# Performance work log

Measured on AMD Instinct MI355X. Metric: run time of the kernel, lower is better.

## Reference

```python
import jax, jax.numpy as jnp
import numpy as np

EPS = 1e-08


def setup_inputs() -> dict:
    key = jax.random.key(0)
    k1, k2 = jax.random.split(key)
    n, d = 8192, 64
    x = jax.random.normal(k1, (n, d), dtype=jnp.float32)
    y = jax.random.randint(k2, (n,), 0, 10, dtype=jnp.int64)
    # weights = 1 / temperature_init = 1 / 0.1
    weights = jnp.full((1,), 10.0, dtype=jnp.float32)
    return {"x": x, "y": y, "weights": weights}


def reference(x, y, weights):
    n = x.shape[0]
    # pairwise euclidean distances (torch.cdist p=2)
    sq = jnp.sum(x * x, axis=1)                      # [n]
    d2 = sq[:, None] + sq[None, :] - 2.0 * (x @ x.T)  # [n,n]
    eye = jnp.eye(n, dtype=bool)
    d2 = jnp.maximum(d2, 0.0)
    dist = jnp.where(eye, 0.0, jnp.sqrt(jnp.where(eye, 1.0, d2)))  # safe sqrt on diag
    expo = jnp.exp(-dist * weights[0])               # [n,n]
    same = (y[:, None] == y[None, :]) & ~eye         # same-class, excluding self
    top = jnp.sum(jnp.where(same, expo, 0.0), axis=1)  # [n]
    bot = jnp.sum(jnp.where(~eye, expo, 0.0), axis=1)  # [n]
    fracs = jnp.log(top / (bot + EPS))
    loss = -jnp.mean(fracs)
    return loss
```

## Files before the change

kernel.cpp:

```cpp
#include <hip/hip_runtime.h>

typedef _Float16 f16x8 __attribute__((ext_vector_type(8)));
typedef float    f32x4 __attribute__((ext_vector_type(4)));

#define N_ROWS 8192
#define DIM 64
#define EPS 1e-8f
#define LOG2E 1.4426950408889634f
#define SHIFT 64.0f
#define SHIFT_LN 44.361419555836499802f
#define TILE_I 256
#define NBI (N_ROWS / TILE_I)
#define TB 512
#define MAXC 17


__global__ void snn_prep(const float* __restrict__ x, _Float16* __restrict__ xh,
                         _Float16* __restrict__ xl, float* __restrict__ sq,
                         float* __restrict__ top, float* __restrict__ bot,
                         float* __restrict__ out) {
    const int gt = blockIdx.x * 256 + threadIdx.x;
    if (gt < N_ROWS) { top[gt] = 0.0f; bot[gt] = 0.0f; }
    if (gt == 0) out[0] = 0.0f;
    const int row = gt >> 6, lane = threadIdx.x & 63;
    float v = x[row * DIM + lane];
    _Float16 h = (_Float16)v;
    _Float16 l = (_Float16)(v - (float)h);
    xh[row * DIM + lane] = h;
    xl[row * DIM + lane] = l;
    float s = v * v;
    #pragma unroll
    for (int off = 32; off > 0; off >>= 1) s += __shfl_xor(s, off, 64);
    if (lane == 0) sq[row] = s;
}

__global__ __launch_bounds__(256, 2) void snn_mfma(
    const _Float16* __restrict__ xh, const _Float16* __restrict__ xl,
    const float* __restrict__ sq, const int* __restrict__ y,
    const float* __restrict__ w,
    float* __restrict__ top, float* __restrict__ bot)
{
    __shared__ float s_sqj[MAXC * 16];
    __shared__ int   s_yj[MAXC * 16];
    __shared__ float s_jt[4][MAXC * 16];
    __shared__ float s_jb[4][MAXC * 16];

    const int bid = blockIdx.x;
    int bi = 0, kk = 0, cum = 0;
    for (int p = 0; p < NBI; p++) {
        int nb = (p < 16) ? p + 1 : p;
        if (bid < cum + nb) { bi = p; kk = bid - cum; break; }
        cum += nb;
    }
    int c0, len;
    if (bi < 16)      { c0 = 16 * kk;            len = 16; }
    else if (kk < 16) { c0 = 17 * kk;            len = 17; }
    else              { c0 = 272 + 16 * (kk - 16); len = 16; }
    const int ndch = min(max(16 * bi - c0, 0), len);
    const int I0 = bi * TILE_I;

    const int tid = threadIdx.x, wv = tid >> 6, lane = tid & 63;
    const int mrow = lane & 15, kq = lane >> 4;

    for (int t = tid; t < len * 16; t += 256) {
        s_sqj[t] = sq[c0 * 16 + t];
        s_yj[t]  = y[c0 * 16 + t];
    }
    __syncthreads();

    const int iw = I0 + wv * 64;

    f16x8 ah[4][2], al[4][2];
    #pragma unroll
    for (int mt = 0; mt < 4; mt++)
        #pragma unroll
        for (int kc = 0; kc < 2; kc++) {
            int a = (iw + mt * 16 + mrow) * DIM + kc * 32 + kq * 8;
            ah[mt][kc] = *(const f16x8*)(xh + a);
            al[mt][kc] = *(const f16x8*)(xl + a);
        }

    float sqi[4][4]; int ypack[4];
    #pragma unroll
    for (int mt = 0; mt < 4; mt++) {
        int yp = 0;
        #pragma unroll
        for (int rr = 0; rr < 4; rr++) {
            int i = iw + mt * 16 + kq * 4 + rr;
            sqi[mt][rr] = sq[i];
            yp |= (y[i] & 255) << (8 * rr);
        }
        ypack[mt] = yp;
    }

    float ts[4][4], bs[4][4];
    #pragma unroll
    for (int mt = 0; mt < 4; mt++)
        #pragma unroll
        for (int rr = 0; rr < 4; rr++) { ts[mt][rr] = 0.0f; bs[mt][rr] = 0.0f; }

    const float c1 = -w[0] * LOG2E;

#define LOAD_B_AND_MFMA()                                                        \
    const int jr = (c0 + ntl) * 16 + mrow;         \
    const int boff = jr * DIM + kq * 8;                                          \
    f16x8 cbh0 = *(const f16x8*)(xh + boff);                                     \
    f16x8 cbh1 = *(const f16x8*)(xh + boff + 32);                                \
    f16x8 cbl0 = *(const f16x8*)(xl + boff);                                     \
    f16x8 cbl1 = *(const f16x8*)(xl + boff + 32);                                \
    const float sqj = s_sqj[ntl * 16 + mrow];                                    \
    const int   yj  = s_yj[ntl * 16 + mrow];                                     \
    f32x4 acc[4];                                                                \
    _Pragma("unroll")                                                            \
    for (int mt = 0; mt < 4; mt++) acc[mt] = (f32x4){0.f, 0.f, 0.f, 0.f};        \
    _Pragma("unroll")                                                            \
    for (int mt = 0; mt < 4; mt++)                                               \
        acc[mt] = __builtin_amdgcn_mfma_f32_16x16x32_f16(ah[mt][0], cbh0, acc[mt], 0, 0, 0); \
    _Pragma("unroll")                                                            \
    for (int mt = 0; mt < 4; mt++)                                               \
        acc[mt] = __builtin_amdgcn_mfma_f32_16x16x32_f16(ah[mt][1], cbh1, acc[mt], 0, 0, 0); \
    _Pragma("unroll")                                                            \
    for (int mt = 0; mt < 4; mt++)                                               \
        acc[mt] = __builtin_amdgcn_mfma_f32_16x16x32_f16(ah[mt][0], cbl0, acc[mt], 0, 0, 0); \
    _Pragma("unroll")                                                            \
    for (int mt = 0; mt < 4; mt++)                                               \
        acc[mt] = __builtin_amdgcn_mfma_f32_16x16x32_f16(ah[mt][1], cbl1, acc[mt], 0, 0, 0); \
    _Pragma("unroll")                                                            \
    for (int mt = 0; mt < 4; mt++)                                               \
        acc[mt] = __builtin_amdgcn_mfma_f32_16x16x32_f16(al[mt][0], cbh0, acc[mt], 0, 0, 0); \
    _Pragma("unroll")                                                            \
    for (int mt = 0; mt < 4; mt++)                                               \
        acc[mt] = __builtin_amdgcn_mfma_f32_16x16x32_f16(al[mt][1], cbh1, acc[mt], 0, 0, 0);

    for (int ntl = 0; ntl < ndch; ntl++) {
        LOAD_B_AND_MFMA()
        float jt = 0.0f, jb = 0.0f;
        #pragma unroll
        for (int mt = 0; mt < 4; mt++)
            #pragma unroll
            for (int rr = 0; rr < 4; rr++) {
                float d2 = fmaf(-2.0f, acc[mt][rr], sqi[mt][rr] + sqj);
                d2 = fmaxf(d2, 0.0f);
                float dist = __builtin_amdgcn_sqrtf(d2);
                float e2 = __builtin_amdgcn_exp2f(fmaf(c1, dist, SHIFT));
                float e2t = (yj == ((ypack[mt] >> (8 * rr)) & 255)) ? e2 : 0.0f;
                ts[mt][rr] += e2t;
                bs[mt][rr] += e2;
                jt += e2t;
                jb += e2;
            }
        jt += __shfl_xor(jt, 16, 64); jt += __shfl_xor(jt, 32, 64);
        jb += __shfl_xor(jb, 16, 64); jb += __shfl_xor(jb, 32, 64);
        if (kq == 0) {
            s_jt[wv][ntl * 16 + mrow] = jt;
            s_jb[wv][ntl * 16 + mrow] = jb;
        }
    }

    for (int ntl = ndch; ntl < len; ntl++) {
        LOAD_B_AND_MFMA()
        #pragma unroll
        for (int mt = 0; mt < 4; mt++)
            #pragma unroll
            for (int rr = 0; rr < 4; rr++) {
                int i = iw + mt * 16 + kq * 4 + rr;
                float d2 = fmaf(-2.0f, acc[mt][rr], sqi[mt][rr] + sqj);
                d2 = fmaxf(d2, 0.0f);
                float dist = __builtin_amdgcn_sqrtf(d2);
                float e2 = __builtin_amdgcn_exp2f(fmaf(c1, dist, SHIFT));
                bool offd = (i != jr);
                bool same = offd && (yj == ((ypack[mt] >> (8 * rr)) & 255));
                bs[mt][rr] += offd ? e2 : 0.0f;
                ts[mt][rr] += same ? e2 : 0.0f;
            }
    }
#undef LOAD_B_AND_MFMA

    #pragma unroll
    for (int mt = 0; mt < 4; mt++)
        #pragma unroll
        for (int rr = 0; rr < 4; rr++) {
            float tv = ts[mt][rr], bv = bs[mt][rr];
            #pragma unroll
            for (int off = 1; off < 16; off <<= 1) {
                tv += __shfl_xor(tv, off, 64);
                bv += __shfl_xor(bv, off, 64);
            }
            if (mrow == 0) {
                int i = iw + mt * 16 + kq * 4 + rr;
                atomicAdd(&top[i], tv);
                atomicAdd(&bot[i], bv);
            }
        }

    if (ndch > 0) {
        __syncthreads();
        for (int t = tid; t < ndch * 16; t += 256) {
            float tt = s_jt[0][t] + s_jt[1][t] + s_jt[2][t] + s_jt[3][t];
            float bb = s_jb[0][t] + s_jb[1][t] + s_jb[2][t] + s_jb[3][t];
            atomicAdd(&top[c0 * 16 + t], tt);
            atomicAdd(&bot[c0 * 16 + t], bb);
        }
    }
}

__global__ __launch_bounds__(256) void snn_final(
    const float* __restrict__ top, const float* __restrict__ bot,
    float* __restrict__ out)
{
    const int i = blockIdx.x * 256 + threadIdx.x;
    float t = top[i];
    float b = bot[i] * 0x1p-64f + EPS;
    float acc = (logf(t) - SHIFT_LN) - logf(b);
    #pragma unroll
    for (int off = 32; off > 0; off >>= 1) acc += __shfl_xor(acc, off, 64);
    __shared__ float red[4];
    if ((threadIdx.x & 63) == 0) red[threadIdx.x >> 6] = acc;
    __syncthreads();
    if (threadIdx.x == 0) {
        float s = red[0] + red[1] + red[2] + red[3];
        atomicAdd(out, -s / (float)N_ROWS);
    }
}

extern "C" void kernel_launch(void* const* d_in, const int* in_sizes, int n_in,
                              void* d_out, int out_size, void* d_ws, size_t ws_size,
                              hipStream_t stream) {
    const float* x = (const float*)d_in[0];
    const int*   y = (const int*)d_in[1];
    const float* w = (const float*)d_in[2];
    float* out = (float*)d_out;

    float* ws  = (float*)d_ws;
    float* top = ws;
    float* bot = ws + N_ROWS;
    float* sq  = ws + 2 * N_ROWS;
    _Float16* xh = (_Float16*)(ws + 3 * N_ROWS);
    _Float16* xl = xh + (size_t)N_ROWS * DIM;

    snn_prep<<<N_ROWS / 4, 256, 0, stream>>>(x, xh, xl, sq, top, bot, out);
    snn_mfma<<<TB, 256, 0, stream>>>(xh, xl, sq, y, w, top, bot);
    snn_final<<<N_ROWS / 256, 256, 0, stream>>>(top, bot, out);
}
```

Baseline: 97.45 us.

## Use 512-row panels with 8-wave blocks and finer column chunking

Raises the row tile from 256 to 512 rows per block, using 512 threads (8 waves), and splits each panel's lower-triangular column range into chunks of at most 9 column tiles. Blocks now come from a per-panel chunk count, which gives 491 blocks. This lets each loaded B column tile be reused by twice as many rows, halving B reloads, and it evens out work per block. The costs are fewer blocks overall and a larger block that needs about four co-resident blocks per CU. Per-wave register use is unchanged, while the shared-memory cross-wave reduction grows to 8 ways.

```diff
diff --git a/kernel.cpp b/kernel.cpp
--- a/kernel.cpp
+++ b/kernel.cpp
@@ -9,10 +9,10 @@
 #define LOG2E 1.4426950408889634f
 #define SHIFT 64.0f
 #define SHIFT_LN 44.361419555836499802f
-#define TILE_I 256
-#define NBI (N_ROWS / TILE_I)
-#define TB 512
-#define MAXC 17
+#define PANEL 512
+#define NPAN (N_ROWS / PANEL)
+#define MAXC 9
+#define TB 491
 
 
 __global__ void snn_prep(const float* __restrict__ x, _Float16* __restrict__ xh,
@@ -34,7 +34,7 @@
     if (lane == 0) sq[row] = s;
 }
 
-__global__ __launch_bounds__(256, 2) void snn_mfma(
+__global__ __launch_bounds__(512, 4) void snn_mfma(
     const _Float16* __restrict__ xh, const _Float16* __restrict__ xl,
     const float* __restrict__ sq, const int* __restrict__ y,
     const float* __restrict__ w,
@@ -42,29 +42,28 @@
 {
     __shared__ float s_sqj[MAXC * 16];
     __shared__ int   s_yj[MAXC * 16];
-    __shared__ float s_jt[4][MAXC * 16];
-    __shared__ float s_jb[4][MAXC * 16];
+    __shared__ float s_jt[8][MAXC * 16];
+    __shared__ float s_jb[8][MAXC * 16];
 
     const int bid = blockIdx.x;
-    int bi = 0, kk = 0, cum = 0;
-    for (int p = 0; p < NBI; p++) {
-        int nb = (p < 16) ? p + 1 : p;
-        if (bid < cum + nb) { bi = p; kk = bid - cum; break; }
+    int p = 0, kk = 0, cum = 0;
+    for (int q = 0; q < NPAN; q++) {
+        int nb = (32 * (q + 1) + MAXC - 1) / MAXC;
+        if (bid < cum + nb) { p = q; kk = bid - cum; break; }
         cum += nb;
     }
-    int c0, len;
-    if (bi < 16)      { c0 = 16 * kk;            len = 16; }
-    else if (kk < 16) { c0 = 17 * kk;            len = 17; }
-    else              { c0 = 272 + 16 * (kk - 16); len = 16; }
-    const int ndch = min(max(16 * bi - c0, 0), len);
-    const int I0 = bi * TILE_I;
+    const int nchunks = 32 * (p + 1);
+    const int lc0 = kk * MAXC;
+    const int len = min(MAXC, nchunks - lc0);
+    const int ndch = min(max(32 * p - lc0, 0), len);
+    const int I0 = p * PANEL;
 
     const int tid = threadIdx.x, wv = tid >> 6, lane = tid & 63;
     const int mrow = lane & 15, kq = lane >> 4;
 
-    for (int t = tid; t < len * 16; t += 256) {
-        s_sqj[t] = sq[c0 * 16 + t];
-        s_yj[t]  = y[c0 * 16 + t];
+    for (int t = tid; t < len * 16; t += 512) {
+        s_sqj[t] = sq[lc0 * 16 + t];
+        s_yj[t]  = y[lc0 * 16 + t];
     }
     __syncthreads();
 
@@ -102,7 +101,7 @@
     const float c1 = -w[0] * LOG2E;
 
 #define LOAD_B_AND_MFMA()                                                        \
-    const int jr = (c0 + ntl) * 16 + mrow;         \
+    const int jr = (lc0 + ntl) * 16 + mrow;        \
     const int boff = jr * DIM + kq * 8;                                          \
     f16x8 cbh0 = *(const f16x8*)(xh + boff);                                     \
     f16x8 cbh1 = *(const f16x8*)(xh + boff + 32);                                \
@@ -195,11 +194,12 @@
 
     if (ndch > 0) {
         __syncthreads();
-        for (int t = tid; t < ndch * 16; t += 256) {
-            float tt = s_jt[0][t] + s_jt[1][t] + s_jt[2][t] + s_jt[3][t];
-            float bb = s_jb[0][t] + s_jb[1][t] + s_jb[2][t] + s_jb[3][t];
-            atomicAdd(&top[c0 * 16 + t], tt);
-            atomicAdd(&bot[c0 * 16 + t], bb);
+        for (int t = tid; t < ndch * 16; t += 512) {
+            float tt = 0.0f, bb = 0.0f;
+            #pragma unroll
+            for (int v = 0; v < 8; v++) { tt += s_jt[v][t]; bb += s_jb[v][t]; }
+            atomicAdd(&top[lc0 * 16 + t], tt);
+            atomicAdd(&bot[lc0 * 16 + t], bb);
         }
     }
 }
@@ -239,6 +239,6 @@
     _Float16* xl = xh + (size_t)N_ROWS * DIM;
 
     snn_prep<<<N_ROWS / 4, 256, 0, stream>>>(x, xh, xl, sq, top, bot, out);
-    snn_mfma<<<TB, 256, 0, stream>>>(xh, xl, sq, y, w, top, bot);
+    snn_mfma<<<TB, 512, 0, stream>>>(xh, xl, sq, y, w, top, bot);
     snn_final<<<N_ROWS / 256, 256, 0, stream>>>(top, bot, out);
 }
```

Result: slower. 194.0 us (+99.0%).
